# Optimization experiments

Hardware: AMD Instinct MI355X
Metric: run time of the kernel (lower is better)

Reference implementation:

```python
import jax, jax.numpy as jnp
import numpy as np

NEG_SLOPE = 0.1

def _leaky(x):
    return jnp.where(x >= 0, x, NEG_SLOPE * x)

def setup_inputs() -> dict:
    key = jax.random.key(0)
    ks = jax.random.split(key, 16)
    B, N, H, W, C = 4, 128, 32, 32, 64
    inp = {
        "image": jax.random.normal(ks[0], (B, 3, H, W), dtype=jnp.float32),
        "coords": jax.random.uniform(ks[1], (B, N, 2), dtype=jnp.float32),
        "w1": jax.random.normal(ks[2], (C, 7), dtype=jnp.float32) * 0.2,
        "b1": jax.random.normal(ks[3], (C,), dtype=jnp.float32) * 0.05,
        "w2": jax.random.normal(ks[4], (C, C), dtype=jnp.float32) * 0.1,
        "b2": jax.random.normal(ks[5], (C,), dtype=jnp.float32) * 0.05,
        "w3": jax.random.normal(ks[6], (C, C), dtype=jnp.float32) * 0.1,
        "b3": jax.random.normal(ks[7], (C,), dtype=jnp.float32) * 0.05,
        "w4": jax.random.normal(ks[8], (C, C), dtype=jnp.float32) * 0.1,
        "b4": jax.random.normal(ks[9], (C,), dtype=jnp.float32) * 0.05,
        "w5": jax.random.normal(ks[10], (C, C), dtype=jnp.float32) * 0.1,
        "b5": jax.random.normal(ks[11], (C,), dtype=jnp.float32) * 0.05,
        "wl": jax.random.normal(ks[12], (3, C), dtype=jnp.float32) * 0.1,
        "bl": jax.random.normal(ks[13], (3,), dtype=jnp.float32) * 0.05,
    }
    return inp

def reference(image, coords, w1, b1, w2, b2, w3, b3, w4, b4, w5, b5, wl, bl):
    B, C_img, H, W = image.shape
    _, N, D = coords.shape
    # position encoding: channel 0 = row/(H-1), channel 1 = col/(W-1)
    row = (jnp.arange(H, dtype=jnp.float32) / (H - 1))[:, None] * jnp.ones((1, W), jnp.float32)
    col = jnp.ones((H, 1), jnp.float32) * (jnp.arange(W, dtype=jnp.float32) / (W - 1))[None, :]
    pos = jnp.stack([row, col], axis=0)  # [2,H,W]
    # x5: [B,5,H,W] = image ++ pos
    x5 = jnp.concatenate([image, jnp.broadcast_to(pos[None], (B, 2, H, W))], axis=1)
    # First 1x1 conv: split weight into image/pos part (5 ch) and coord part (2 ch);
    # avoids materializing the expanded [B*N,7,H,W] input (same math as conv on concat).
    img_part = jnp.einsum('oc,bchw->bohw', w1[:, :5], x5)          # [B,c,H,W]
    crd_part = jnp.einsum('od,bnd->bno', w1[:, 5:], coords)         # [B,N,c]
    h = _leaky(img_part[:, None] + crd_part[:, :, :, None, None] + b1[None, None, :, None, None])  # [B,N,c,H,W]
    for wi, bi in ((w2, b2), (w3, b3), (w4, b4), (w5, b5)):
        h = _leaky(jnp.einsum('oc,bnchw->bnohw', wi, h) + bi[None, None, :, None, None])
    pooled = jnp.mean(h, axis=(-2, -1))                             # [B,N,c] (AdaptiveAvgPool2d(1,1)+Flatten)
    pred = jax.nn.sigmoid(jnp.einsum('oc,bnc->bno', wl, pooled) + bl)  # [B,N,3]
    return jnp.transpose(pred, (0, 2, 1))                           # [B,3,N]
```

## Files before the change

kernel.cpp:

```cpp
#include <hip/hip_runtime.h>
#include <math.h>


typedef float  f32x4  __attribute__((ext_vector_type(4)));
typedef f32x4  f32x4a __attribute__((may_alias));
typedef __bf16 bf16x8 __attribute__((ext_vector_type(8)));
typedef bf16x8 bf16x8a __attribute__((may_alias));
typedef __bf16 bf16x4 __attribute__((ext_vector_type(4)));
typedef bf16x4 bf16x4a __attribute__((may_alias));
typedef float  floata __attribute__((may_alias));

#define MFMA16(a, b, c) __builtin_amdgcn_mfma_f32_16x16x32_bf16((a), (b), (c), 0, 0, 0)

#define WL_H    0
#define ACT_H   18432

__global__ __launch_bounds__(256, 2) void mlp_mfma_kernel(
    const float* __restrict__ image,
    const float* __restrict__ coords,
    const float* __restrict__ w1, const float* __restrict__ b1,
    const float* __restrict__ w2, const float* __restrict__ b2,
    const float* __restrict__ w3, const float* __restrict__ b3,
    const float* __restrict__ w4, const float* __restrict__ b4,
    const float* __restrict__ w5, const float* __restrict__ b5,
    const float* __restrict__ wl, const float* __restrict__ bl,
    float* __restrict__ out)
{
    __shared__ __align__(16) __bf16 LDSH[18432 + 16384];
    __shared__ __align__(16) float  BL[320];

    const int tid  = threadIdx.x;
    const int wave = tid >> 6;
    const int lane = tid & 63;
    const int c15  = lane & 15;
    const int q    = lane >> 4;
    const int bn   = blockIdx.x;
    const int b    = bn >> 7;

    const float qm = (q == 0) ? 1.0f : 0.0f;

    const float* Ws[4] = {w2, w3, w4, w5};

    #pragma unroll 1
    for (int i = 0; i < 9; ++i) {
        const int id = wave + i * 4;
        __bf16* dst = &LDSH[WL_H + id * 512 + lane * 8];
        if (id < 32) {
            const int l  = id >> 3;
            const int mt = (id >> 1) & 3;
            const int ks = id & 1;
            const float* src = Ws[l] + (mt * 16 + c15) * 64 + ks * 32 + q * 8;
            f32x4 lo = *(const f32x4a*)src;
            f32x4 hi = *(const f32x4a*)(src + 4);
            bf16x8 f;
            f[0] = (__bf16)lo[0]; f[1] = (__bf16)lo[1];
            f[2] = (__bf16)lo[2]; f[3] = (__bf16)lo[3];
            f[4] = (__bf16)hi[0]; f[5] = (__bf16)hi[1];
            f[6] = (__bf16)hi[2]; f[7] = (__bf16)hi[3];
            *(bf16x8a*)dst = f;
        } else {
            const int mt = id - 32;
            bf16x8 f;
            #pragma unroll
            for (int j = 0; j < 7; ++j)
                f[j] = (__bf16)(qm * w1[(mt * 16 + c15) * 7 + j]);
            f[7] = (__bf16)0.0f;
            *(bf16x8a*)dst = f;
        }
    }
    if (tid < 64) {
        BL[tid]       = b1[tid];
        BL[64 + tid]  = b2[tid];
        BL[128 + tid] = b3[tid];
        BL[192 + tid] = b4[tid];
        BL[256 + tid] = b5[tid];
    }
    __syncthreads();

    const float cx = coords[2 * bn + 0];
    const float cy = coords[2 * bn + 1];
    const float* img = image + b * 3072;

    __bf16* Xw = &LDSH[ACT_H + wave * 4096];
    const int lane_woff = c15 * 8 + (q >> 1) * 128 + (q & 1) * 4;

    f32x4 pool[4];
    #pragma unroll
    for (int mt = 0; mt < 4; ++mt) pool[mt] = (f32x4){0.f, 0.f, 0.f, 0.f};

    bf16x8 a1[4];
    #pragma unroll
    for (int mt = 0; mt < 4; ++mt)
        a1[mt] = *(const bf16x8a*)&LDSH[WL_H + (32 + mt) * 512 + lane * 8];

    float pix[2][2][3];
    #pragma unroll
    for (int g = 0; g < 2; ++g)
        #pragma unroll
        for (int ntl = 0; ntl < 2; ++ntl) {
            const int hw = wave * 256 + g * 32 + ntl * 16 + c15;
            pix[g][ntl][0] = img[hw];
            pix[g][ntl][1] = img[1024 + hw];
            pix[g][ntl][2] = img[2048 + hw];
        }

    auto store_tile = [&](f32x4 (&acc)[4][2], int g) {
        #pragma unroll
        for (int mt = 0; mt < 4; ++mt)
            #pragma unroll
            for (int ntl = 0; ntl < 2; ++ntl) {
                f32x4 a = acc[mt][ntl];
                bf16x4 p;
                #pragma unroll
                for (int r = 0; r < 4; ++r) {
                    float v = fmaxf(a[r], 0.1f * a[r]);
                    p[r] = (__bf16)v;
                }
                const int off = g * 2048 + (ntl * 2 + (mt >> 1)) * 512
                              + (mt & 1) * 256 + lane_woff;
                *(bf16x4a*)&Xw[off] = p;
            }
    };

    #pragma unroll 1
    for (int t = 0; t < 4; ++t) {
        {
            f32x4 bv[4];
            #pragma unroll
            for (int mt = 0; mt < 4; ++mt)
                bv[mt] = *(const f32x4a*)&BL[mt * 16 + 4 * q];

            #pragma unroll
            for (int g = 0; g < 2; ++g) {
                bf16x8 bft[2];
                #pragma unroll
                for (int ntl = 0; ntl < 2; ++ntl) {
                    const int hw = wave * 256 + t * 64 + g * 32 + ntl * 16 + c15;
                    bf16x8 f;
                    f[0] = (__bf16)(qm * pix[g][ntl][0]);
                    f[1] = (__bf16)(qm * pix[g][ntl][1]);
                    f[2] = (__bf16)(qm * pix[g][ntl][2]);
                    f[3] = (__bf16)(qm * (float)(hw >> 5) * (1.0f / 31.0f));
                    f[4] = (__bf16)(qm * (float)(hw & 31) * (1.0f / 31.0f));
                    f[5] = (__bf16)(qm * cx);
                    f[6] = (__bf16)(qm * cy);
                    f[7] = (__bf16)0.0f;
                    bft[ntl] = f;
                }
                f32x4 acc[4][2];
                #pragma unroll
                for (int mt = 0; mt < 4; ++mt) {
                    acc[mt][0] = bv[mt]; acc[mt][1] = bv[mt];
                }
                #pragma unroll
                for (int mt = 0; mt < 4; ++mt)
                    #pragma unroll
                    for (int ntl = 0; ntl < 2; ++ntl)
                        acc[mt][ntl] = MFMA16(a1[mt], bft[ntl], acc[mt][ntl]);
                store_tile(acc, g);
            }
        }

        if (t < 3) {
            #pragma unroll
            for (int g = 0; g < 2; ++g)
                #pragma unroll
                for (int ntl = 0; ntl < 2; ++ntl) {
                    const int hw = wave * 256 + (t + 1) * 64 + g * 32 + ntl * 16 + c15;
                    pix[g][ntl][0] = img[hw];
                    pix[g][ntl][1] = img[1024 + hw];
                    pix[g][ntl][2] = img[2048 + hw];
                }
        }

        #pragma unroll
        for (int l = 0; l < 4; ++l) {
            bf16x8 af[4][2];
            #pragma unroll
            for (int mt = 0; mt < 4; ++mt)
                #pragma unroll
                for (int ks = 0; ks < 2; ++ks)
                    af[mt][ks] = *(const bf16x8a*)
                        &LDSH[WL_H + (l * 8 + mt * 2 + ks) * 512 + lane * 8];
            f32x4 bv[4];
            #pragma unroll
            for (int mt = 0; mt < 4; ++mt)
                bv[mt] = *(const f32x4a*)&BL[(l + 1) * 64 + mt * 16 + 4 * q];

            #pragma unroll
            for (int g = 0; g < 2; ++g) {
                bf16x8 bf[2][2];
                #pragma unroll
                for (int ntl = 0; ntl < 2; ++ntl)
                    #pragma unroll
                    for (int ks = 0; ks < 2; ++ks)
                        bf[ntl][ks] = *(const bf16x8a*)
                            &Xw[g * 2048 + ((ntl * 2 + ks) * 64 + lane) * 8];
                f32x4 acc[4][2];
                #pragma unroll
                for (int mt = 0; mt < 4; ++mt) {
                    acc[mt][0] = bv[mt]; acc[mt][1] = bv[mt];
                }
                #pragma unroll
                for (int mt = 0; mt < 4; ++mt)
                    #pragma unroll
                    for (int ntl = 0; ntl < 2; ++ntl)
                        #pragma unroll
                        for (int ks = 0; ks < 2; ++ks)
                            acc[mt][ntl] = MFMA16(af[mt][ks], bf[ntl][ks], acc[mt][ntl]);
                if (l < 3) {
                    store_tile(acc, g);
                } else {
                    #pragma unroll
                    for (int mt = 0; mt < 4; ++mt)
                        #pragma unroll
                        for (int ntl = 0; ntl < 2; ++ntl) {
                            f32x4 a = acc[mt][ntl];
                            #pragma unroll
                            for (int r = 0; r < 4; ++r)
                                pool[mt][r] += fmaxf(a[r], 0.1f * a[r]);
                        }
                }
            }
        }
    }

    floata* Xf = (floata*)Xw;
    #pragma unroll
    for (int mt = 0; mt < 4; ++mt)
        #pragma unroll
        for (int r = 0; r < 4; ++r)
            Xf[(mt * 16 + 4 * q + r) * 16 + c15] = pool[mt][r];

    __syncthreads();

    if (tid < 64) {
        const int c = tid;
        float s = 0.0f;
        #pragma unroll
        for (int w = 0; w < 4; ++w) {
            const floata* P = (const floata*)&LDSH[ACT_H + w * 4096];
            #pragma unroll
            for (int c4 = 0; c4 < 4; ++c4) {
                f32x4 v = *(const f32x4a*)&P[c * 16 + c4 * 4];
                s += v[0] + v[1] + v[2] + v[3];
            }
        }
        const float p = s * (1.0f / 1024.0f);
        float s0 = wl[c] * p;
        float s1 = wl[64 + c] * p;
        float s2 = wl[128 + c] * p;
        #pragma unroll
        for (int off = 32; off > 0; off >>= 1) {
            s0 += __shfl_down(s0, off, 64);
            s1 += __shfl_down(s1, off, 64);
            s2 += __shfl_down(s2, off, 64);
        }
        if (c == 0) {
            const int n = bn & 127;
            out[(b * 3 + 0) * 128 + n] = 1.0f / (1.0f + expf(-(bl[0] + s0)));
            out[(b * 3 + 1) * 128 + n] = 1.0f / (1.0f + expf(-(bl[1] + s1)));
            out[(b * 3 + 2) * 128 + n] = 1.0f / (1.0f + expf(-(bl[2] + s2)));
        }
    }
}

extern "C" void kernel_launch(void* const* d_in, const int* in_sizes, int n_in,
                              void* d_out, int out_size, void* d_ws, size_t ws_size,
                              hipStream_t stream) {
    const float* image  = (const float*)d_in[0];
    const float* coords = (const float*)d_in[1];
    const float* w1 = (const float*)d_in[2];
    const float* b1 = (const float*)d_in[3];
    const float* w2 = (const float*)d_in[4];
    const float* b2 = (const float*)d_in[5];
    const float* w3 = (const float*)d_in[6];
    const float* b3 = (const float*)d_in[7];
    const float* w4 = (const float*)d_in[8];
    const float* b4 = (const float*)d_in[9];
    const float* w5 = (const float*)d_in[10];
    const float* b5 = (const float*)d_in[11];
    const float* wl = (const float*)d_in[12];
    const float* bl = (const float*)d_in[13];
    float* out = (float*)d_out;

    mlp_mfma_kernel<<<dim3(512), dim3(256), 0, stream>>>(
        image, coords, w1, b1, w2, b2, w3, b3, w4, b4, w5, b5, wl, bl, out);
}
```

Baseline: 109.4 us.

## Chain MLP layers in registers via 16x16x16 MFMA, removing LDS activation round-trips

Switches from the 16x16x32 to the 16x16x16 bf16 MFMA, whose accumulator layout matches the B-operand layout, so each layer's output can feed the next layer directly from registers. Before, activations were written to and read back from LDS between layers. All four 64x64 weight matrices are now held in registers (64 bf16x4 fragments per lane), and each wave processes 16 pixels per iteration over 16 iterations. The first layer uses a packed K=16 input with zero-padded weights. The cost is heavy register pressure, which may reduce occupancy or cause spills under launch_bounds(256,2), and a smaller N tile per iteration.

```diff
diff --git a/kernel.cpp b/kernel.cpp
--- a/kernel.cpp
+++ b/kernel.cpp
@@ -4,16 +4,22 @@
 
 typedef float  f32x4  __attribute__((ext_vector_type(4)));
 typedef f32x4  f32x4a __attribute__((may_alias));
-typedef __bf16 bf16x8 __attribute__((ext_vector_type(8)));
-typedef bf16x8 bf16x8a __attribute__((may_alias));
 typedef __bf16 bf16x4 __attribute__((ext_vector_type(4)));
 typedef bf16x4 bf16x4a __attribute__((may_alias));
+typedef short  s16x4  __attribute__((ext_vector_type(4)));
 typedef float  floata __attribute__((may_alias));
 
-#define MFMA16(a, b, c) __builtin_amdgcn_mfma_f32_16x16x32_bf16((a), (b), (c), 0, 0, 0)
-
-#define WL_H    0
-#define ACT_H   18432
+static __device__ __forceinline__ f32x4 MFMA16(bf16x4 a, bf16x4 b, f32x4 c) {
+    return __builtin_amdgcn_mfma_f32_16x16x16bf16_1k(
+        __builtin_bit_cast(s16x4, a), __builtin_bit_cast(s16x4, b), c, 0, 0, 0);
+}
+
+static __device__ __forceinline__ bf16x4 cvt4(f32x4 v) {
+    bf16x4 r;
+    r[0] = (__bf16)v[0]; r[1] = (__bf16)v[1];
+    r[2] = (__bf16)v[2]; r[3] = (__bf16)v[3];
+    return r;
+}
 
 __global__ __launch_bounds__(256, 2) void mlp_mfma_kernel(
     const float* __restrict__ image,
@@ -26,8 +32,9 @@
     const float* __restrict__ wl, const float* __restrict__ bl,
     float* __restrict__ out)
 {
-    __shared__ __align__(16) __bf16 LDSH[18432 + 16384];
-    __shared__ __align__(16) float  BL[320];
+    __shared__ __align__(16) __bf16 WF[16384];
+    __shared__ __align__(16) float  POOL[4][1024];
+    __shared__ float BL[320];
 
     const int tid  = threadIdx.x;
     const int wave = tid >> 6;
@@ -37,35 +44,15 @@
     const int bn   = blockIdx.x;
     const int b    = bn >> 7;
 
-    const float qm = (q == 0) ? 1.0f : 0.0f;
-
     const float* Ws[4] = {w2, w3, w4, w5};
 
-    #pragma unroll 1
-    for (int i = 0; i < 9; ++i) {
-        const int id = wave + i * 4;
-        __bf16* dst = &LDSH[WL_H + id * 512 + lane * 8];
-        if (id < 32) {
-            const int l  = id >> 3;
-            const int mt = (id >> 1) & 3;
-            const int ks = id & 1;
-            const float* src = Ws[l] + (mt * 16 + c15) * 64 + ks * 32 + q * 8;
-            f32x4 lo = *(const f32x4a*)src;
-            f32x4 hi = *(const f32x4a*)(src + 4);
-            bf16x8 f;
-            f[0] = (__bf16)lo[0]; f[1] = (__bf16)lo[1];
-            f[2] = (__bf16)lo[2]; f[3] = (__bf16)lo[3];
-            f[4] = (__bf16)hi[0]; f[5] = (__bf16)hi[1];
-            f[6] = (__bf16)hi[2]; f[7] = (__bf16)hi[3];
-            *(bf16x8a*)dst = f;
-        } else {
-            const int mt = id - 32;
-            bf16x8 f;
-            #pragma unroll
-            for (int j = 0; j < 7; ++j)
-                f[j] = (__bf16)(qm * w1[(mt * 16 + c15) * 7 + j]);
-            f[7] = (__bf16)0.0f;
-            *(bf16x8a*)dst = f;
+    {
+        const float* Wsrc = Ws[wave];
+        #pragma unroll
+        for (int f = 0; f < 16; ++f) {
+            const int mt = f >> 2, ks = f & 3;
+            f32x4 v = *(const f32x4a*)(Wsrc + (mt * 16 + c15) * 64 + ks * 16 + 4 * q);
+            *(bf16x4a*)&WF[((wave * 16 + f) * 64 + lane) * 4] = cvt4(v);
         }
     }
     if (tid < 64) {
@@ -77,155 +64,102 @@
     }
     __syncthreads();
 
+    bf16x4 wf[4][4][4];
+    #pragma unroll
+    for (int l = 0; l < 4; ++l)
+        #pragma unroll
+        for (int mt = 0; mt < 4; ++mt)
+            #pragma unroll
+            for (int ks = 0; ks < 4; ++ks)
+                wf[l][mt][ks] = *(const bf16x4a*)
+                    &WF[((l * 16 + mt * 4 + ks) * 64 + lane) * 4];
+
+    bf16x4 a1[4];
+    #pragma unroll
+    for (int mt = 0; mt < 4; ++mt)
+        #pragma unroll
+        for (int j = 0; j < 4; ++j) {
+            const int k = 4 * q + j;
+            float v = (k < 7) ? w1[(mt * 16 + c15) * 7 + k] : 0.0f;
+            a1[mt][j] = (__bf16)v;
+        }
+
     const float cx = coords[2 * bn + 0];
     const float cy = coords[2 * bn + 1];
     const float* img = image + b * 3072;
 
-    __bf16* Xw = &LDSH[ACT_H + wave * 4096];
-    const int lane_woff = c15 * 8 + (q >> 1) * 128 + (q & 1) * 4;
+    const float inv31 = 1.0f / 31.0f;
+    const bool  q0  = (q == 0);
+    const float g0e = (q == 1) ? (float)c15 * inv31        : 0.0f;
+    const float g0o = (q == 1) ? (float)(c15 + 16) * inv31 : 0.0f;
+    const float g1  = (q == 1) ? cx : 0.0f;
+    const float g2  = (q == 1) ? cy : 0.0f;
 
     f32x4 pool[4];
     #pragma unroll
     for (int mt = 0; mt < 4; ++mt) pool[mt] = (f32x4){0.f, 0.f, 0.f, 0.f};
 
-    bf16x8 a1[4];
-    #pragma unroll
-    for (int mt = 0; mt < 4; ++mt)
-        a1[mt] = *(const bf16x8a*)&LDSH[WL_H + (32 + mt) * 512 + lane * 8];
-
-    float pix[2][2][3];
-    #pragma unroll
-    for (int g = 0; g < 2; ++g)
-        #pragma unroll
-        for (int ntl = 0; ntl < 2; ++ntl) {
-            const int hw = wave * 256 + g * 32 + ntl * 16 + c15;
-            pix[g][ntl][0] = img[hw];
-            pix[g][ntl][1] = img[1024 + hw];
-            pix[g][ntl][2] = img[2048 + hw];
-        }
-
-    auto store_tile = [&](f32x4 (&acc)[4][2], int g) {
-        #pragma unroll
-        for (int mt = 0; mt < 4; ++mt)
-            #pragma unroll
-            for (int ntl = 0; ntl < 2; ++ntl) {
-                f32x4 a = acc[mt][ntl];
-                bf16x4 p;
+    float p0, p1, p2;
+    {
+        const int hw = wave * 256 + c15;
+        p0 = img[hw]; p1 = img[1024 + hw]; p2 = img[2048 + hw];
+    }
+
+    #pragma unroll 1
+    for (int t = 0; t < 16; ++t) {
+        const float rowv = (float)(wave * 8 + (t >> 1)) * inv31;
+        const float f0 = q0 ? p0 : ((t & 1) ? g0o : g0e);
+        const float f1 = q0 ? p1 : g1;
+        const float f2 = q0 ? p2 : g2;
+        const float f3 = q0 ? rowv : 0.0f;
+        bf16x4 B1;
+        B1[0] = (__bf16)f0; B1[1] = (__bf16)f1;
+        B1[2] = (__bf16)f2; B1[3] = (__bf16)f3;
+
+        {
+            const int tt = (t < 15) ? (t + 1) : 15;
+            const int hw = wave * 256 + tt * 16 + c15;
+            p0 = img[hw]; p1 = img[1024 + hw]; p2 = img[2048 + hw];
+        }
+
+        f32x4 acc[4];
+        #pragma unroll
+        for (int mt = 0; mt < 4; ++mt)
+            acc[mt] = *(const f32x4a*)&BL[mt * 16 + 4 * q];
+        #pragma unroll
+        for (int mt = 0; mt < 4; ++mt)
+            acc[mt] = MFMA16(a1[mt], B1, acc[mt]);
+
+        bf16x4 Bf[4];
+        #pragma unroll
+        for (int l = 0; l < 4; ++l) {
+            #pragma unroll
+            for (int mt = 0; mt < 4; ++mt) {
+                f32x4 v = acc[mt];
                 #pragma unroll
-                for (int r = 0; r < 4; ++r) {
-                    float v = fmaxf(a[r], 0.1f * a[r]);
-                    p[r] = (__bf16)v;
-                }
-                const int off = g * 2048 + (ntl * 2 + (mt >> 1)) * 512
-                              + (mt & 1) * 256 + lane_woff;
-                *(bf16x4a*)&Xw[off] = p;
+                for (int r = 0; r < 4; ++r) v[r] = fmaxf(v[r], 0.1f * v[r]);
+                Bf[mt] = cvt4(v);
             }
-    };
-
-    #pragma unroll 1
-    for (int t = 0; t < 4; ++t) {
-        {
-            f32x4 bv[4];
             #pragma unroll
             for (int mt = 0; mt < 4; ++mt)
-                bv[mt] = *(const f32x4a*)&BL[mt * 16 + 4 * q];
-
-            #pragma unroll
-            for (int g = 0; g < 2; ++g) {
-                bf16x8 bft[2];
-                #pragma unroll
-                for (int ntl = 0; ntl < 2; ++ntl) {
-                    const int hw = wave * 256 + t * 64 + g * 32 + ntl * 16 + c15;
-                    bf16x8 f;
-                    f[0] = (__bf16)(qm * pix[g][ntl][0]);
-                    f[1] = (__bf16)(qm * pix[g][ntl][1]);
-                    f[2] = (__bf16)(qm * pix[g][ntl][2]);
-                    f[3] = (__bf16)(qm * (float)(hw >> 5) * (1.0f / 31.0f));
-                    f[4] = (__bf16)(qm * (float)(hw & 31) * (1.0f / 31.0f));
-                    f[5] = (__bf16)(qm * cx);
-                    f[6] = (__bf16)(qm * cy);
-                    f[7] = (__bf16)0.0f;
-                    bft[ntl] = f;
-                }
-                f32x4 acc[4][2];
-                #pragma unroll
-                for (int mt = 0; mt < 4; ++mt) {
-                    acc[mt][0] = bv[mt]; acc[mt][1] = bv[mt];
-                }
+                acc[mt] = *(const f32x4a*)&BL[(l + 1) * 64 + mt * 16 + 4 * q];
+            #pragma unroll
+            for (int ks = 0; ks < 4; ++ks)
                 #pragma unroll
                 for (int mt = 0; mt < 4; ++mt)
-                    #pragma unroll
-                    for (int ntl = 0; ntl < 2; ++ntl)
-                        acc[mt][ntl] = MFMA16(a1[mt], bft[ntl], acc[mt][ntl]);
-                store_tile(acc, g);
+                    acc[mt] = MFMA16(wf[l][mt][ks], Bf[ks], acc[mt]);
+        }
+
+        #pragma unroll
+        for (int mt = 0; mt < 4; ++mt)
+            #pragma unroll
+            for (int r = 0; r < 4; ++r) {
+                const float v = acc[mt][r];
+                pool[mt][r] += fmaxf(v, 0.1f * v);
             }
-        }
-
-        if (t < 3) {
-            #pragma unroll
-            for (int g = 0; g < 2; ++g)
-                #pragma unroll
-                for (int ntl = 0; ntl < 2; ++ntl) {
-                    const int hw = wave * 256 + (t + 1) * 64 + g * 32 + ntl * 16 + c15;
-                    pix[g][ntl][0] = img[hw];
-                    pix[g][ntl][1] = img[1024 + hw];
-                    pix[g][ntl][2] = img[2048 + hw];
-                }
-        }
-
-        #pragma unroll
-        for (int l = 0; l < 4; ++l) {
-            bf16x8 af[4][2];
-            #pragma unroll
-            for (int mt = 0; mt < 4; ++mt)
-                #pragma unroll
-                for (int ks = 0; ks < 2; ++ks)
-                    af[mt][ks] = *(const bf16x8a*)
-                        &LDSH[WL_H + (l * 8 + mt * 2 + ks) * 512 + lane * 8];
-            f32x4 bv[4];
-            #pragma unroll
-            for (int mt = 0; mt < 4; ++mt)
-                bv[mt] = *(const f32x4a*)&BL[(l + 1) * 64 + mt * 16 + 4 * q];
-
-            #pragma unroll
-            for (int g = 0; g < 2; ++g) {
-                bf16x8 bf[2][2];
-                #pragma unroll
-                for (int ntl = 0; ntl < 2; ++ntl)
-                    #pragma unroll
-                    for (int ks = 0; ks < 2; ++ks)
-                        bf[ntl][ks] = *(const bf16x8a*)
-                            &Xw[g * 2048 + ((ntl * 2 + ks) * 64 + lane) * 8];
-                f32x4 acc[4][2];
-                #pragma unroll
-                for (int mt = 0; mt < 4; ++mt) {
-                    acc[mt][0] = bv[mt]; acc[mt][1] = bv[mt];
-                }
-                #pragma unroll
-                for (int mt = 0; mt < 4; ++mt)
-                    #pragma unroll
-                    for (int ntl = 0; ntl < 2; ++ntl)
-                        #pragma unroll
-                        for (int ks = 0; ks < 2; ++ks)
-                            acc[mt][ntl] = MFMA16(af[mt][ks], bf[ntl][ks], acc[mt][ntl]);
-                if (l < 3) {
-                    store_tile(acc, g);
-                } else {
-                    #pragma unroll
-                    for (int mt = 0; mt < 4; ++mt)
-                        #pragma unroll
-                        for (int ntl = 0; ntl < 2; ++ntl) {
-                            f32x4 a = acc[mt][ntl];
-                            #pragma unroll
-                            for (int r = 0; r < 4; ++r)
-                                pool[mt][r] += fmaxf(a[r], 0.1f * a[r]);
-                        }
-                }
-            }
-        }
-    }
-
-    floata* Xf = (floata*)Xw;
+    }
+
+    floata* Xf = &POOL[wave][0];
     #pragma unroll
     for (int mt = 0; mt < 4; ++mt)
         #pragma unroll
@@ -239,7 +173,7 @@
         float s = 0.0f;
         #pragma unroll
         for (int w = 0; w < 4; ++w) {
-            const floata* P = (const floata*)&LDSH[ACT_H + w * 4096];
+            const floata* P = &POOL[w][0];
             #pragma unroll
             for (int c4 = 0; c4 < 4; ++c4) {
                 f32x4 v = *(const f32x4a*)&P[c * 16 + c4 * 4];
```

Measured after the change: 132.2 us. 1.21x slower.
